# Optimization experiments

Hardware: AMD Instinct MI355X
Metric: run time of the kernel (lower is better)

The kernel has to match this reference:

```python
import jax, jax.numpy as jnp
from jax import lax
import numpy as np

B, T, D, H, P = 2048, 256, 128, 256, 2048


def setup_inputs() -> dict:
    key = jax.random.key(0)
    ks = jax.random.split(key, 6)
    s_ih = 1.0 / np.sqrt(H)  # PyTorch GRU init scale
    return {
        "x": jax.random.normal(ks[0], (B, T, D), dtype=jnp.float32),
        "w_ih": jax.random.uniform(ks[1], (3 * H, D), minval=-s_ih, maxval=s_ih, dtype=jnp.float32),
        "w_hh": jax.random.uniform(ks[2], (3 * H, H), minval=-s_ih, maxval=s_ih, dtype=jnp.float32),
        "b_ih": jax.random.uniform(ks[3], (3 * H,), minval=-s_ih, maxval=s_ih, dtype=jnp.float32),
        "b_hh": jax.random.uniform(ks[4], (3 * H,), minval=-s_ih, maxval=s_ih, dtype=jnp.float32),
        "prototypes": jax.random.normal(ks[5], (P, H), dtype=jnp.float32),
    }


def _gru_last_hidden(x, w_ih, w_hh, b_ih, b_hh):
    # Precompute all input projections in one big GEMM: [B, T, 3H]
    x_proj = jnp.einsum("btd,gd->btg", x, w_ih) + b_ih
    h0 = jnp.zeros((x.shape[0], w_hh.shape[1]), x.dtype)

    def step(h, xp):
        hp = h @ w_hh.T + b_hh                       # [B, 3H]
        xr, xz, xn = jnp.split(xp, 3, axis=-1)       # gate order: r, z, n (PyTorch)
        hr, hz, hn = jnp.split(hp, 3, axis=-1)
        r = jax.nn.sigmoid(xr + hr)
        z = jax.nn.sigmoid(xz + hz)
        n = jnp.tanh(xn + r * hn)
        h = (1.0 - z) * n + z * h
        return h, None

    h_last, _ = lax.scan(step, h0, jnp.swapaxes(x_proj, 0, 1))  # scan over time
    return h_last  # [B, H]


def _cdist(h, prototypes):
    # Euclidean distance via ||h||^2 + ||p||^2 - 2 h.p^T (same math as torch.cdist p=2)
    d2 = (
        jnp.sum(h * h, axis=1, keepdims=True)
        + jnp.sum(prototypes * prototypes, axis=1)
        - 2.0 * (h @ prototypes.T)
    )
    return jnp.sqrt(jnp.maximum(d2, 0.0))  # [B, P]


def reference(x, w_ih, w_hh, b_ih, b_hh, prototypes):
    h_last = _gru_last_hidden(x, w_ih, w_hh, b_ih, b_hh)
    dists = _cdist(h_last, prototypes)
    assignments = jnp.argmin(dists, axis=1)  # [B] int
    return assignments
```

## Files before the change

### kernel.cpp

```cpp
#include <hip/hip_runtime.h>

#define TT 256
#define DD 128
#define HH 256
#define PP 2048
#define RB 16
#define NBLK 128
#define NTH 1024

typedef _Float16 half8 __attribute__((ext_vector_type(8)));
typedef _Float16 half4 __attribute__((ext_vector_type(4)));
typedef float f32x4 __attribute__((ext_vector_type(4)));

#define MFMA16(a, b, c) __builtin_amdgcn_mfma_f32_16x16x32_f16((a), (b), (c), 0, 0, 0)
#define INV2048 (4.8828125e-4f)

__device__ __forceinline__ float sigmoidf_(float v) { return 1.0f / (1.0f + expf(-v)); }

__global__ void prep_kernel(const float* __restrict__ w_ih, const float* __restrict__ w_hh,
                            const float* __restrict__ protos,
                            _Float16* __restrict__ WF, float* __restrict__ pT) {
    int f = blockIdx.x * blockDim.x + threadIdx.x;
    if (f < 294912) {
        int s = f / 24576, rem = f % 24576;
        int tt = rem / 512, rem2 = rem % 512;
        int m = rem2 >> 5, kl = rem2 & 31;
        int grow = (tt % 3) * 256 + (tt / 3) * 16 + m;
        float v = (s < 4) ? w_ih[grow * DD + s * 32 + kl]
                          : w_hh[grow * HH + (s - 4) * 32 + kl];
        _Float16 hi = (_Float16)v;
        _Float16 lo = (_Float16)((v - (float)hi) * 2048.0f);
        int lane = m + 16 * (kl >> 3);
        int base = ((s * 2 + 0) * 48 + tt) * 512 + lane * 8 + (kl & 7);
        WF[base] = hi;
        WF[base + 48 * 512] = lo;
    }
    if (f < HH * PP) pT[f] = protos[(f & (PP - 1)) * HH + (f >> 11)];
}

__launch_bounds__(NTH)
__global__ void gru_kernel(const float* __restrict__ x,
                           const _Float16* __restrict__ WF,
                           const float* __restrict__ b_ih, const float* __restrict__ b_hh,
                           const float* __restrict__ pT,
                           int* __restrict__ out) {
    __shared__ __align__(16) _Float16 fragB[2 * 24 * 512];
    __shared__ float hsF[HH * RB];
    __shared__ float redv[16][RB];
    __shared__ int   redi[16][RB];
#define FRAG(b, sec) (fragB + ((b) * 24 + (sec)) * 512)

    const int tid  = threadIdx.x;
    const int lane = tid & 63;
    const int w    = tid >> 6;
    const int row0 = blockIdx.x * RB;
    const int lane8 = lane * 8;
    const int t0w   = 3 * w;

    float bRv[4], bZv[4], bXNv[4], bHNv[4];
    #pragma unroll
    for (int r = 0; r < 4; ++r) {
        const int j = 16 * w + ((lane >> 4) << 2) + r;
        bRv[r]  = b_ih[j] + b_hh[j];
        bZv[r]  = b_ih[HH + j] + b_hh[HH + j];
        bXNv[r] = b_ih[2 * HH + j];
        bHNv[r] = b_hh[2 * HH + j];
    }

    float hprev[4] = {0.f, 0.f, 0.f, 0.f};

    const int xn = tid >> 5, xk0 = (tid & 31) * 4;
    const float* const xrow = x + (size_t)(row0 + (xn & 15)) * TT * DD + xk0;
    const int xsec = 2 * (xk0 >> 5);
    const int xidx = (((xk0 & 31) >> 3) * 16 + (xn & 15)) * 8 + (xk0 & 7);

    if (tid < 512) {
        const float4 v = *(const float4*)xrow;
        const float vv[4] = {v.x, v.y, v.z, v.w};
        _Float16 xh[4], xl[4];
        #pragma unroll
        for (int u = 0; u < 4; ++u) {
            xh[u] = (_Float16)vv[u];
            xl[u] = (_Float16)((vv[u] - (float)xh[u]) * 2048.0f);
        }
        *(half4*)(FRAG(0, xsec) + xidx)     = half4{xh[0], xh[1], xh[2], xh[3]};
        *(half4*)(FRAG(0, xsec + 1) + xidx) = half4{xl[0], xl[1], xl[2], xl[3]};
        _Float16* hz = FRAG(0, 8);
        const half8 z8 = {};
        *(half8*)(hz + tid * 16)     = z8;
        *(half8*)(hz + tid * 16 + 8) = z8;
    }
    __syncthreads();

    const half8* __restrict__ WH = (const half8*)WF;

    for (int t = 0; t < TT; ++t) {
        const int cur = t & 1, nxtb = cur ^ 1;

        float4 pfx = make_float4(0.f, 0.f, 0.f, 0.f);
        const bool havepf = (t + 1 < TT) && (tid < 512);
        if (havepf) pfx = *(const float4*)(xrow + (size_t)(t + 1) * DD);

        f32x4 aM[3], aX[3], aMh, aXh;
        #pragma unroll
        for (int i = 0; i < 3; ++i) { aM[i] = f32x4{0.f,0.f,0.f,0.f}; aX[i] = f32x4{0.f,0.f,0.f,0.f}; }
        aMh = f32x4{0.f,0.f,0.f,0.f}; aXh = f32x4{0.f,0.f,0.f,0.f};

        #pragma unroll 2
        for (int s = 0; s < 4; ++s) {
            const half8 bh = *(const half8*)(FRAG(cur, 2 * s) + lane8);
            const half8 bl = *(const half8*)(FRAG(cur, 2 * s + 1) + lane8);
            #pragma unroll
            for (int i = 0; i < 3; ++i) {
                const half8 wh = WH[((2 * s) * 48 + t0w + i) * 64 + lane];
                const half8 wl = WH[((2 * s + 1) * 48 + t0w + i) * 64 + lane];
                aM[i] = MFMA16(wh, bh, aM[i]);
                aX[i] = MFMA16(wh, bl, aX[i]);
                aX[i] = MFMA16(wl, bh, aX[i]);
            }
        }
        #pragma unroll 2
        for (int s = 4; s < 12; ++s) {
            const half8 bh = *(const half8*)(FRAG(cur, 2 * s) + lane8);
            const half8 bl = *(const half8*)(FRAG(cur, 2 * s + 1) + lane8);
            #pragma unroll
            for (int i = 0; i < 3; ++i) {
                const half8 wh = WH[((2 * s) * 48 + t0w + i) * 64 + lane];
                const half8 wl = WH[((2 * s + 1) * 48 + t0w + i) * 64 + lane];
                if (i == 2) {
                    aMh = MFMA16(wh, bh, aMh);
                    aXh = MFMA16(wh, bl, aXh);
                    aXh = MFMA16(wl, bh, aXh);
                } else {
                    aM[i] = MFMA16(wh, bh, aM[i]);
                    aX[i] = MFMA16(wh, bl, aX[i]);
                    aX[i] = MFMA16(wl, bh, aX[i]);
                }
            }
        }

        {
            _Float16 hh_[4], hl_[4];
            #pragma unroll
            for (int r = 0; r < 4; ++r) {
                const float sR  = aM[0][r] + aX[0][r] * INV2048 + bRv[r];
                const float sZ  = aM[1][r] + aX[1][r] * INV2048 + bZv[r];
                const float sXN = aM[2][r] + aX[2][r] * INV2048 + bXNv[r];
                const float sHN = aMh[r]   + aXh[r]   * INV2048 + bHNv[r];
                const float Rg = sigmoidf_(sR);
                const float Zg = sigmoidf_(sZ);
                const float Ng = tanhf(sXN + Rg * sHN);
                const float h = (1.0f - Zg) * Ng + Zg * hprev[r];
                hprev[r] = h;
                hh_[r] = (_Float16)h;
                hl_[r] = (_Float16)((h - (float)hh_[r]) * 2048.0f);
            }
            const int jb  = 16 * w + ((lane >> 4) << 2);
            const int sec = 2 * (4 + (jb >> 5));
            const int idx = (((jb & 31) >> 3) * 16 + (lane & 15)) * 8 + (jb & 7);
            *(half4*)(FRAG(nxtb, sec) + idx)     = half4{hh_[0], hh_[1], hh_[2], hh_[3]};
            *(half4*)(FRAG(nxtb, sec + 1) + idx) = half4{hl_[0], hl_[1], hl_[2], hl_[3]};
        }

        if (havepf) {
            const float vv[4] = {pfx.x, pfx.y, pfx.z, pfx.w};
            _Float16 xh[4], xl[4];
            #pragma unroll
            for (int u = 0; u < 4; ++u) {
                xh[u] = (_Float16)vv[u];
                xl[u] = (_Float16)((vv[u] - (float)xh[u]) * 2048.0f);
            }
            *(half4*)(FRAG(nxtb, xsec) + xidx)     = half4{xh[0], xh[1], xh[2], xh[3]};
            *(half4*)(FRAG(nxtb, xsec + 1) + xidx) = half4{xl[0], xl[1], xl[2], xl[3]};
        }
        __syncthreads();
    }

    #pragma unroll
    for (int r = 0; r < 4; ++r) {
        const int j = 16 * w + ((lane >> 4) << 2) + r;
        hsF[j * RB + (lane & 15)] = hprev[r];
    }
    __syncthreads();

    float bv[16]; int bi[16];
    #pragma unroll
    for (int r = 0; r < 16; ++r) { bv[r] = 3.4e38f; bi[r] = 0; }
    for (int m = 0; m < 2; ++m) {
        const int p = m * 1024 + tid;
        float d2[16];
        #pragma unroll
        for (int r = 0; r < 16; ++r) d2[r] = 0.f;
        #pragma unroll 2
        for (int k = 0; k < HH; ++k) {
            const float pv = pT[(size_t)k * PP + p];
            #pragma unroll
            for (int g4 = 0; g4 < 4; ++g4) {
                const float4 hv = *(const float4*)&hsF[k * RB + g4 * 4];
                float d;
                d = hv.x - pv; d2[g4 * 4 + 0] += d * d;
                d = hv.y - pv; d2[g4 * 4 + 1] += d * d;
                d = hv.z - pv; d2[g4 * 4 + 2] += d * d;
                d = hv.w - pv; d2[g4 * 4 + 3] += d * d;
            }
        }
        #pragma unroll
        for (int r = 0; r < 16; ++r)
            if (d2[r] < bv[r]) { bv[r] = d2[r]; bi[r] = p; }
    }
    #pragma unroll
    for (int s = 1; s < 64; s <<= 1) {
        #pragma unroll
        for (int r = 0; r < 16; ++r) {
            const float ov = __shfl_xor(bv[r], s);
            const int   oi = __shfl_xor(bi[r], s);
            if (ov < bv[r] || (ov == bv[r] && oi < bi[r])) { bv[r] = ov; bi[r] = oi; }
        }
    }
    if (lane == 0) {
        #pragma unroll
        for (int r = 0; r < 16; ++r) { redv[w][r] = bv[r]; redi[w][r] = bi[r]; }
    }
    __syncthreads();
    if (tid < RB) {
        float v = redv[0][tid]; int idx = redi[0][tid];
        #pragma unroll
        for (int u = 1; u < 16; ++u) {
            const float ov = redv[u][tid]; const int oi = redi[u][tid];
            if (ov < v || (ov == v && oi < idx)) { v = ov; idx = oi; }
        }
        out[row0 + tid] = idx;
    }
}

extern "C" void kernel_launch(void* const* d_in, const int* in_sizes, int n_in,
                              void* d_out, int out_size, void* d_ws, size_t ws_size,
                              hipStream_t stream) {
    const float* x      = (const float*)d_in[0];
    const float* w_ih   = (const float*)d_in[1];
    const float* w_hh   = (const float*)d_in[2];
    const float* b_ih   = (const float*)d_in[3];
    const float* b_hh   = (const float*)d_in[4];
    const float* protos = (const float*)d_in[5];
    int* out = (int*)d_out;

    _Float16* WF = (_Float16*)d_ws;
    float*    pT = (float*)((char*)d_ws + 589824 * sizeof(_Float16));

    hipLaunchKernelGGL(prep_kernel, dim3((HH * PP + 255) / 256), dim3(256), 0, stream,
                       w_ih, w_hh, protos, WF, pT);
    hipLaunchKernelGGL(gru_kernel, dim3(NBLK), dim3(NTH), 0, stream,
                       x, WF, b_ih, b_hh, pT, out);
}
```

Before: 2.952 ms.

## Use fast intrinsic gate activations and stagger per-wave k-section order

Swaps the sigmoid and tanh gate activations for __expf plus hardware reciprocal approximations, cutting transcendental instruction cost inside the serial recurrence. Also merges the x-section and h-section MFMA loops into one loop whose starting section is rotated per wave, so waves read different LDS fragments at the same time and bank contention is reduced. The rotation adds a runtime branch on the section type and modular indexing, and the approximate math may slightly change the hidden state and, near ties, the argmin assignments.

Result: faster. 2.477 ms (median of 2 runs) (-16.1%).

```diff
diff --git a/kernel.cpp b/kernel.cpp
--- a/kernel.cpp
+++ b/kernel.cpp
@@ -15,7 +15,13 @@
 #define MFMA16(a, b, c) __builtin_amdgcn_mfma_f32_16x16x32_f16((a), (b), (c), 0, 0, 0)
 #define INV2048 (4.8828125e-4f)
 
-__device__ __forceinline__ float sigmoidf_(float v) { return 1.0f / (1.0f + expf(-v)); }
+__device__ __forceinline__ float fast_sigmoid(float v) {
+    return __builtin_amdgcn_rcpf(1.0f + __expf(-v));
+}
+__device__ __forceinline__ float fast_tanh(float v) {
+    const float e2 = __expf(2.0f * v);
+    return 1.0f - 2.0f * __builtin_amdgcn_rcpf(e2 + 1.0f);
+}
 
 __global__ void prep_kernel(const float* __restrict__ w_ih, const float* __restrict__ w_hh,
                             const float* __restrict__ protos,
@@ -56,6 +62,7 @@
     const int row0 = blockIdx.x * RB;
     const int lane8 = lane * 8;
     const int t0w   = 3 * w;
+    const int sw    = (w >= 12) ? (w - 12) : w;
 
     float bRv[4], bZv[4], bXNv[4], bHNv[4];
     #pragma unroll
@@ -107,34 +114,23 @@
         aMh = f32x4{0.f,0.f,0.f,0.f}; aXh = f32x4{0.f,0.f,0.f,0.f};
 
         #pragma unroll 2
-        for (int s = 0; s < 4; ++s) {
+        for (int i = 0; i < 12; ++i) {
+            int s = sw + i; if (s >= 12) s -= 12;
             const half8 bh = *(const half8*)(FRAG(cur, 2 * s) + lane8);
             const half8 bl = *(const half8*)(FRAG(cur, 2 * s + 1) + lane8);
-            #pragma unroll
-            for (int i = 0; i < 3; ++i) {
-                const half8 wh = WH[((2 * s) * 48 + t0w + i) * 64 + lane];
-                const half8 wl = WH[((2 * s + 1) * 48 + t0w + i) * 64 + lane];
-                aM[i] = MFMA16(wh, bh, aM[i]);
-                aX[i] = MFMA16(wh, bl, aX[i]);
-                aX[i] = MFMA16(wl, bh, aX[i]);
-            }
-        }
-        #pragma unroll 2
-        for (int s = 4; s < 12; ++s) {
-            const half8 bh = *(const half8*)(FRAG(cur, 2 * s) + lane8);
-            const half8 bl = *(const half8*)(FRAG(cur, 2 * s + 1) + lane8);
-            #pragma unroll
-            for (int i = 0; i < 3; ++i) {
-                const half8 wh = WH[((2 * s) * 48 + t0w + i) * 64 + lane];
-                const half8 wl = WH[((2 * s + 1) * 48 + t0w + i) * 64 + lane];
-                if (i == 2) {
+            const bool isX = (s < 4);
+            #pragma unroll
+            for (int i2 = 0; i2 < 3; ++i2) {
+                const half8 wh = WH[((2 * s) * 48 + t0w + i2) * 64 + lane];
+                const half8 wl = WH[((2 * s + 1) * 48 + t0w + i2) * 64 + lane];
+                if (i2 == 2 && !isX) {
                     aMh = MFMA16(wh, bh, aMh);
                     aXh = MFMA16(wh, bl, aXh);
                     aXh = MFMA16(wl, bh, aXh);
                 } else {
-                    aM[i] = MFMA16(wh, bh, aM[i]);
-                    aX[i] = MFMA16(wh, bl, aX[i]);
-                    aX[i] = MFMA16(wl, bh, aX[i]);
+                    aM[i2] = MFMA16(wh, bh, aM[i2]);
+                    aX[i2] = MFMA16(wh, bl, aX[i2]);
+                    aX[i2] = MFMA16(wl, bh, aX[i2]);
                 }
             }
         }
@@ -147,9 +143,9 @@
                 const float sZ  = aM[1][r] + aX[1][r] * INV2048 + bZv[r];
                 const float sXN = aM[2][r] + aX[2][r] * INV2048 + bXNv[r];
                 const float sHN = aMh[r]   + aXh[r]   * INV2048 + bHNv[r];
-                const float Rg = sigmoidf_(sR);
-                const float Zg = sigmoidf_(sZ);
-                const float Ng = tanhf(sXN + Rg * sHN);
+                const float Rg = fast_sigmoid(sR);
+                const float Zg = fast_sigmoid(sZ);
+                const float Ng = fast_tanh(sXN + Rg * sHN);
                 const float h = (1.0f - Zg) * Ng + Zg * hprev[r];
                 hprev[r] = h;
                 hh_[r] = (_Float16)h;
```
